# Kernel tuning notes

Hardware: AMD Instinct MI355X
Metric: run time of the kernel (lower is better)

## Reference

```python
import jax, jax.numpy as jnp
import numpy as np

K = 5          # reassembly kernel size
S = 2          # scale factor
ENC_PAD = 1    # encoder_kernel_size // 2


def _conv2d(x, w, pad):
    return jax.lax.conv_general_dilated(
        x, w, window_strides=(1, 1), padding=[(pad, pad), (pad, pad)],
        dimension_numbers=('NCHW', 'OIHW', 'NCHW'))


def setup_inputs() -> dict:
    key = jax.random.key(0)
    k1, k2, k3 = jax.random.split(key, 3)
    x = jax.random.normal(k1, (2, 256, 40, 40), dtype=jnp.float32)
    # channel compressor: xavier-uniform-ish 1x1 conv weight (64, 256, 1, 1)
    limit = np.sqrt(6.0 / (256 + 64)).astype(np.float32)
    w_comp = jax.random.uniform(k2, (64, 256, 1, 1), dtype=jnp.float32,
                                minval=-limit, maxval=limit)
    # content encoder: normal(0, 0.001), out = k^2*s^2 = 100 channels
    w_enc = 0.001 * jax.random.normal(k3, (100, 64, 3, 3), dtype=jnp.float32)
    return {"x": x, "w_comp": w_comp, "w_enc": w_enc}


def reference(x, w_comp, w_enc):
    b, c, h, w = x.shape
    k2 = K * K
    h_up, w_up = h * S, w * S

    # --- kernel prediction ---
    compressed = _conv2d(x, w_comp, 0)                # (b, 64, h, w)
    kern = _conv2d(compressed, w_enc, ENC_PAD)        # (b, k2*S^2, h, w)
    # pixel shuffle: (b, k2, S, S, h, w) -> (b, k2, h, S, w, S) -> (b, k2, h_up, w_up)
    kern = kern.reshape(b, k2, S, S, h, w).transpose(0, 1, 4, 2, 5, 3)
    kern = kern.reshape(b, k2, h_up * w_up)
    kern = jax.nn.softmax(kern, axis=1)               # softmax over k2

    # --- unfold (im2col, padding K//2) ---
    pad = K // 2
    xp = jnp.pad(x, ((0, 0), (0, 0), (pad, pad), (pad, pad)))
    # (b, c, k2, h, w): channel-major, kernel offsets inner (matches torch F.unfold)
    patches = jnp.stack([xp[:, :, i:i + h, j:j + w]
                         for i in range(K) for j in range(K)], axis=2)
    x_unfold = patches.reshape(b, c, k2, h * w)

    # --- reassembly (faithful to the torch 'efficient' path) ---
    # torch repeat_interleaves x_unfold S^2 times along the h*w axis and
    # multiplies with kernels flattened in (h_up*w_up) row-major order; that
    # pairing is exactly kern reshaped to (b, k2, h*w, S^2):
    kern4 = kern.reshape(b, k2, h * w, S * S)
    out = jnp.einsum('bckp,bkpd->bcpd', x_unfold, kern4)  # (b, c, h*w, S^2)
    return out.reshape(b, c, h_up, w_up)
```

## Files before the change

### kernel.cpp

```cpp
#include <hip/hip_runtime.h>

#define B   2
#define C   256
#define CM  64
#define CE  100
#define H   40
#define W   40
#define HW  1600
#define KK  25

__global__ __launch_bounds__(256) void k1_fused(
    const float* __restrict__ x, const float* __restrict__ w_comp,
    const float* __restrict__ w_enc, float* __restrict__ pc,
    float* __restrict__ xpad, float* __restrict__ wT) {
  const int bid = blockIdx.x;
  const int tid = threadIdx.x;

  if (bid >= 712) {
    int idx = (bid - 712) * 256 + tid;
    if (idx < 57600) {
      int row = idx / 576, col = idx - row * 576;
      int ocq = row / 25, ol = row - ocq * 25;
      wT[((size_t)(ocq * 576 + col)) * 32 + ol] = w_enc[idx];
    }
    return;
  }
  if (bid >= 200) {
    const int plane = bid - 200;
    const float* src = x + (size_t)plane * HW;
    float* dst = xpad + (size_t)plane * (44 * 48);
    for (int i = tid; i < 44 * 48; i += 256) {
      int py = i / 48, px = i - py * 48;
      int gy = py - 2, gx = px - 2;
      float v = 0.f;
      if (gy >= 0 && gy < H && gx >= 0 && gx < W) v = src[gy * W + gx];
      dst[i] = v;
    }
    return;
  }

  const int t = bid % 25, ich = (bid / 25) & 3, b = bid / 100;
  __shared__ __align__(16) float xs[64 * 64];
  __shared__ __align__(16) float wsA[64 * 64];

  const float4* x4 = (const float4*)(x + ((size_t)b * C + ich * 64) * HW + t * 64);
#pragma unroll
  for (int i = 0; i < 4; i++) {
    int idx = tid + i * 256;
    ((float4*)xs)[idx] = x4[(idx >> 4) * 400 + (idx & 15)];
  }
  const float4* w4 = (const float4*)w_comp;
#pragma unroll
  for (int i = 0; i < 4; i++) {
    int idx = tid + i * 256;
    int icq = idx >> 6, oc = idx & 63;
    float4 f = w4[oc * 64 + ich * 16 + icq];
    wsA[(icq * 4 + 0) * 64 + oc] = f.x;
    wsA[(icq * 4 + 1) * 64 + oc] = f.y;
    wsA[(icq * 4 + 2) * 64 + oc] = f.z;
    wsA[(icq * 4 + 3) * 64 + oc] = f.w;
  }
  __syncthreads();

  const int ty = tid >> 4, tx = tid & 15;
  float acc[4][4];
#pragma unroll
  for (int i = 0; i < 4; i++)
#pragma unroll
    for (int j = 0; j < 4; j++) acc[i][j] = 0.f;

#pragma unroll 4
  for (int icl = 0; icl < 64; icl++) {
    float4 a = *(const float4*)&wsA[icl * 64 + ty * 4];
    float4 bb = *(const float4*)&xs[icl * 64 + tx * 4];
    float av[4] = {a.x, a.y, a.z, a.w};
    float bv[4] = {bb.x, bb.y, bb.z, bb.w};
#pragma unroll
    for (int i = 0; i < 4; i++)
#pragma unroll
      for (int j = 0; j < 4; j++) acc[i][j] += av[i] * bv[j];
  }

  float* o = pc + ((size_t)ich * B + b) * CM * HW + t * 64 + tx * 4;
#pragma unroll
  for (int j = 0; j < 4; j++)
    *(float4*)&o[(size_t)(ty * 4 + j) * HW] =
        make_float4(acc[j][0], acc[j][1], acc[j][2], acc[j][3]);
}

__global__ __launch_bounds__(256) void k2_conv3x3(
    const float* __restrict__ pc, const float* __restrict__ wT,
    float* __restrict__ encP) {
  const int t = blockIdx.x, ocq = blockIdx.y, icq = blockIdx.z;
  const int ty = t / 10, tx = t - ty * 10;
  __shared__ __align__(16) float smem[3200];
  float* cs   = smem;
  float* pacc = smem;
  const int tid = threadIdx.x;

  for (int i = tid; i < 1920; i += 256) {
    int bb = i / 960, r = i - bb * 960;
    int icl = r / 60, rr = r - icl * 60;
    int yy = rr / 6, xx = rr - yy * 6;
    int gy = ty * 8 + yy - 1, gx = tx * 4 + xx - 1;
    float v = 0.f;
    if (gy >= 0 && gy < H && gx >= 0 && gx < W) {
      int o = bb * 102400 + (icq * 16 + icl) * HW + gy * W + gx;
      v = pc[o] + pc[204800 + o] + pc[409600 + o] + pc[614400 + o];
    }
    cs[i] = v;
  }
  __syncthreads();

  const int wv = tid >> 6, lane = tid & 63;
  const int bb = lane >> 5, py = (lane & 31) >> 2, px = lane & 3;
  float acc[25];
#pragma unroll
  for (int j = 0; j < 25; j++) acc[j] = 0.f;

  const float* wbase0 = wT + (size_t)((ocq * 4 + icq) * 16) * 288;

#pragma unroll
  for (int t4 = 0; t4 < 4; t4++) {
    const int icl = __builtin_amdgcn_readfirstlane(wv * 4 + t4);
    const float* c0 = &cs[(bb * 16 + icl) * 60 + py * 6 + px];
    const float* wrow = wbase0 + icl * 288;
#pragma unroll
    for (int dy = 0; dy < 3; dy++)
#pragma unroll
      for (int dx = 0; dx < 3; dx++) {
        const float xv = c0[dy * 6 + dx];
        const float* wq = wrow + (dy * 3 + dx) * 32;
#pragma unroll
        for (int j = 0; j < 25; j++) acc[j] = fmaf(xv, wq[j], acc[j]);
      }
  }

  __syncthreads();
  if (wv == 1 || wv == 3) {
    const int slot = wv >> 1;
#pragma unroll
    for (int j = 0; j < 25; j++) pacc[(slot * 25 + j) * 64 + lane] = acc[j];
  }
  __syncthreads();
  if (wv == 0 || wv == 2) {
    const int slot = wv >> 1;
#pragma unroll
    for (int j = 0; j < 25; j++) acc[j] += pacc[(slot * 25 + j) * 64 + lane];
  }
  __syncthreads();
  if (wv == 2) {
#pragma unroll
    for (int j = 0; j < 25; j++) pacc[j * 64 + lane] = acc[j];
  }
  __syncthreads();
  if (wv == 0) {
    const int base_px = (ty * 8 + py) * W + tx * 4 + px;
#pragma unroll
    for (int ol = 0; ol < 25; ol++)
      encP[(((size_t)icq * 2 + bb) * CE + ocq * 25 + ol) * HW + base_px] =
          acc[ol] + pacc[ol * 64 + lane];
  }
}

__global__ __launch_bounds__(256) void k3_fused(
    const float* __restrict__ xpad, const float* __restrict__ encP,
    float* __restrict__ out) {
  const int i0 = blockIdx.x;
  const int jq = blockIdx.y;
  const int b  = blockIdx.z;
  const int tid = threadIdx.x;

  __shared__ __align__(16) float xsm[40 * 260];
  __shared__ __align__(16) float sv[400];
  __shared__ __align__(16) float wlds[400];

  const int t20 = (jq >= 5) ? 1 : 0;
  if (tid < 200) {
    const float* eb = encP + (size_t)b * 160000 + i0 * 40;
#pragma unroll
    for (int u = 0; u < 2; u++) {
      const int p = tid * 2 + u;
      const int k = p >> 4, v = p & 15;
      const int j0l = v >> 2, d = v & 3;
      const int off = 2 * t20 + (d & 1);
      const int col = (jq * 4 + j0l - 20 * t20) * 2 + (d >> 1);
      const float* ep = eb + (size_t)(k * 4 + off) * 1600 + col;
      sv[p] = ep[0] + ep[320000] + ep[640000] + ep[960000];
    }
  }

  {
    const float* xb = xpad + (size_t)b * 256 * (44 * 48) + i0 * 48 + jq * 4;
    const int f4 = tid & 1, cth = tid >> 1;
#pragma unroll
    for (int it = 0; it < 10; it++) {
      const int ki = (it < 5) ? it : it - 5;
      const int c  = (it < 5 ? 0 : 128) + cth;
      float4 v = *(const float4*)(xb + ((size_t)c * 44 + ki) * 48 + f4 * 4);
      const int px = ki * 8 + f4 * 4;
      xsm[(px + 0) * 260 + c] = v.x;
      xsm[(px + 1) * 260 + c] = v.y;
      xsm[(px + 2) * 260 + c] = v.z;
      xsm[(px + 3) * 260 + c] = v.w;
    }
  }
  __syncthreads();

  if (tid < 16) {
    const int j0l = tid >> 2, d = tid & 3;
    float vk[KK];
    float m = -1e30f;
#pragma unroll
    for (int k = 0; k < KK; k++) {
      vk[k] = sv[k * 16 + tid];
      m = fmaxf(m, vk[k]);
    }
    float s = 0.f;
#pragma unroll
    for (int k = 0; k < KK; k++) {
      vk[k] = expf(vk[k] - m);
      s += vk[k];
    }
    const float inv = 1.f / s;
#pragma unroll
    for (int k = 0; k < KK; k++) wlds[j0l * 100 + k * 4 + d] = vk[k] * inv;
  }
  __syncthreads();

  const int wv = tid >> 6, lane = tid & 63, ch0 = lane * 4;
  float4 a0 = make_float4(0.f, 0.f, 0.f, 0.f);
  float4 a1 = a0, a2 = a0, a3 = a0;

#pragma unroll
  for (int ki = 0; ki < 5; ki++)
#pragma unroll
    for (int kj = 0; kj < 5; kj++) {
      float4 xv = *(const float4*)&xsm[(ki * 8 + wv + kj) * 260 + ch0];
      float4 w4 = *(const float4*)&wlds[wv * 100 + (ki * 5 + kj) * 4];
      a0.x += xv.x * w4.x; a0.y += xv.y * w4.x; a0.z += xv.z * w4.x; a0.w += xv.w * w4.x;
      a1.x += xv.x * w4.y; a1.y += xv.y * w4.y; a1.z += xv.z * w4.y; a1.w += xv.w * w4.y;
      a2.x += xv.x * w4.z; a2.y += xv.y * w4.z; a2.z += xv.z * w4.z; a2.w += xv.w * w4.z;
      a3.x += xv.x * w4.w; a3.y += xv.y * w4.w; a3.z += xv.z * w4.w; a3.w += xv.w * w4.w;
    }

  const int j0 = jq * 4 + wv;
  float* ob = out + ((size_t)b * C + ch0) * 6400 + i0 * 160 + j0 * 4;
  *(float4*)&ob[0]     = make_float4(a0.x, a1.x, a2.x, a3.x);
  *(float4*)&ob[6400]  = make_float4(a0.y, a1.y, a2.y, a3.y);
  *(float4*)&ob[12800] = make_float4(a0.z, a1.z, a2.z, a3.z);
  *(float4*)&ob[19200] = make_float4(a0.w, a1.w, a2.w, a3.w);
}

extern "C" void kernel_launch(void* const* d_in, const int* in_sizes, int n_in,
                              void* d_out, int out_size, void* d_ws, size_t ws_size,
                              hipStream_t stream) {
  const float* x      = (const float*)d_in[0];
  const float* w_comp = (const float*)d_in[1];
  const float* w_enc  = (const float*)d_in[2];
  float* out = (float*)d_out;

  float* pc    = (float*)d_ws;
  float* encP  = (float*)((char*)d_ws + 3276800);
  float* wT    = (float*)((char*)d_ws + 8396800);
  float* xpad  = (float*)((char*)d_ws + 8691712);

  k1_fused<<<dim3(937), 256, 0, stream>>>(x, w_comp, w_enc, pc, xpad, wT);
  k2_conv3x3<<<dim3(50, 4, 4), 256, 0, stream>>>(pc, wT, encP);
  k3_fused<<<dim3(40, 10, B), 256, 0, stream>>>(xpad, encP, out);
}
```

Baseline: 103.4 us.

## Fuse three kernels into one persistent kernel with atomic grid barriers

Merges the compressor/pad/weight-transpose, 3x3 encoder conv, and softmax-reassembly kernels into a single persistent kernel of 400 blocks. Blocks loop over virtual block indices and meet at atomic-counter grid barriers between stages. A memset resets the barrier counters on each call. The aim is to remove the launch gaps between kernels, at the cost of spin-wait barriers, a deadlock risk if not all blocks are co-resident, and a larger shared-memory footprint that may lower occupancy.

```diff
diff --git a/kernel.cpp b/kernel.cpp
--- a/kernel.cpp
+++ b/kernel.cpp
@@ -9,247 +9,259 @@
 #define HW  1600
 #define KK  25
 
-__global__ __launch_bounds__(256) void k1_fused(
+#define NBLK 400u
+
+__device__ __forceinline__ void grid_barrier(unsigned* cnt) {
+  __syncthreads();
+  if (threadIdx.x == 0) {
+    __hip_atomic_fetch_add(cnt, 1u, __ATOMIC_RELEASE, __HIP_MEMORY_SCOPE_AGENT);
+    while (__hip_atomic_load(cnt, __ATOMIC_ACQUIRE, __HIP_MEMORY_SCOPE_AGENT) <
+           NBLK)
+      __builtin_amdgcn_s_sleep(2);
+  }
+  __syncthreads();
+}
+
+__global__ __launch_bounds__(256) void k_all(
     const float* __restrict__ x, const float* __restrict__ w_comp,
     const float* __restrict__ w_enc, float* __restrict__ pc,
-    float* __restrict__ xpad, float* __restrict__ wT) {
+    float* __restrict__ encP, float* __restrict__ wT,
+    float* __restrict__ xpad, float* __restrict__ out,
+    unsigned* __restrict__ bars) {
+  __shared__ __align__(16) float smem[11200];
   const int bid = blockIdx.x;
   const int tid = threadIdx.x;
 
-  if (bid >= 712) {
-    int idx = (bid - 712) * 256 + tid;
-    if (idx < 57600) {
-      int row = idx / 576, col = idx - row * 576;
-      int ocq = row / 25, ol = row - ocq * 25;
-      wT[((size_t)(ocq * 576 + col)) * 32 + ol] = w_enc[idx];
-    }
-    return;
-  }
-  if (bid >= 200) {
-    const int plane = bid - 200;
-    const float* src = x + (size_t)plane * HW;
-    float* dst = xpad + (size_t)plane * (44 * 48);
-    for (int i = tid; i < 44 * 48; i += 256) {
-      int py = i / 48, px = i - py * 48;
-      int gy = py - 2, gx = px - 2;
+  for (int vb = bid; vb < 937; vb += NBLK) {
+    if (vb >= 712) {
+      int idx = (vb - 712) * 256 + tid;
+      if (idx < 57600) {
+        int row = idx / 576, col = idx - row * 576;
+        int ocq = row / 25, ol = row - ocq * 25;
+        wT[((size_t)(ocq * 576 + col)) * 32 + ol] = w_enc[idx];
+      }
+    } else if (vb >= 200) {
+      const int plane = vb - 200;
+      const float* src = x + (size_t)plane * HW;
+      float* dst = xpad + (size_t)plane * (44 * 48);
+      for (int i = tid; i < 44 * 48; i += 256) {
+        int py = i / 48, px = i - py * 48;
+        int gy = py - 2, gx = px - 2;
+        float v = 0.f;
+        if (gy >= 0 && gy < H && gx >= 0 && gx < W) v = src[gy * W + gx];
+        dst[i] = v;
+      }
+    } else {
+      const int t = vb % 25, ich = (vb / 25) & 3, b = vb / 100;
+      float* xs  = smem;
+      float* wsA = smem + 4096;
+
+      const float4* x4 =
+          (const float4*)(x + ((size_t)b * C + ich * 64) * HW + t * 64);
+#pragma unroll
+      for (int i = 0; i < 4; i++) {
+        int idx = tid + i * 256;
+        ((float4*)xs)[idx] = x4[(idx >> 4) * 400 + (idx & 15)];
+      }
+      const float4* w4 = (const float4*)w_comp;
+#pragma unroll
+      for (int i = 0; i < 4; i++) {
+        int idx = tid + i * 256;
+        int icq = idx >> 6, oc = idx & 63;
+        float4 f = w4[oc * 64 + ich * 16 + icq];
+        wsA[(icq * 4 + 0) * 64 + oc] = f.x;
+        wsA[(icq * 4 + 1) * 64 + oc] = f.y;
+        wsA[(icq * 4 + 2) * 64 + oc] = f.z;
+        wsA[(icq * 4 + 3) * 64 + oc] = f.w;
+      }
+      __syncthreads();
+
+      const int ty = tid >> 4, tx = tid & 15;
+      float acc[4][4];
+#pragma unroll
+      for (int i = 0; i < 4; i++)
+#pragma unroll
+        for (int j = 0; j < 4; j++) acc[i][j] = 0.f;
+
+#pragma unroll 4
+      for (int icl = 0; icl < 64; icl++) {
+        float4 a = *(const float4*)&wsA[icl * 64 + ty * 4];
+        float4 bb = *(const float4*)&xs[icl * 64 + tx * 4];
+        float av[4] = {a.x, a.y, a.z, a.w};
+        float bv[4] = {bb.x, bb.y, bb.z, bb.w};
+#pragma unroll
+        for (int i = 0; i < 4; i++)
+#pragma unroll
+          for (int j = 0; j < 4; j++) acc[i][j] += av[i] * bv[j];
+      }
+
+      float* o = pc + ((size_t)ich * B + b) * CM * HW + t * 64 + tx * 4;
+#pragma unroll
+      for (int j = 0; j < 4; j++)
+        *(float4*)&o[(size_t)(ty * 4 + j) * HW] =
+            make_float4(acc[j][0], acc[j][1], acc[j][2], acc[j][3]);
+    }
+  }
+
+  grid_barrier(&bars[0]);
+
+  for (int vb = bid; vb < 800; vb += NBLK) {
+    __syncthreads();
+    const int t = vb % 50, ocq = (vb / 50) % 4, icq = vb / 200;
+    const int ty = t / 10, tx = t - ty * 10;
+    float* cs   = smem;
+    float* pacc = smem;
+
+    for (int i = tid; i < 1920; i += 256) {
+      int bb = i / 960, r = i - bb * 960;
+      int icl = r / 60, rr = r - icl * 60;
+      int yy = rr / 6, xx = rr - yy * 6;
+      int gy = ty * 8 + yy - 1, gx = tx * 4 + xx - 1;
       float v = 0.f;
-      if (gy >= 0 && gy < H && gx >= 0 && gx < W) v = src[gy * W + gx];
-      dst[i] = v;
-    }
-    return;
-  }
-
-  const int t = bid % 25, ich = (bid / 25) & 3, b = bid / 100;
-  __shared__ __align__(16) float xs[64 * 64];
-  __shared__ __align__(16) float wsA[64 * 64];
-
-  const float4* x4 = (const float4*)(x + ((size_t)b * C + ich * 64) * HW + t * 64);
-#pragma unroll
-  for (int i = 0; i < 4; i++) {
-    int idx = tid + i * 256;
-    ((float4*)xs)[idx] = x4[(idx >> 4) * 400 + (idx & 15)];
-  }
-  const float4* w4 = (const float4*)w_comp;
-#pragma unroll
-  for (int i = 0; i < 4; i++) {
-    int idx = tid + i * 256;
-    int icq = idx >> 6, oc = idx & 63;
-    float4 f = w4[oc * 64 + ich * 16 + icq];
-    wsA[(icq * 4 + 0) * 64 + oc] = f.x;
-    wsA[(icq * 4 + 1) * 64 + oc] = f.y;
-    wsA[(icq * 4 + 2) * 64 + oc] = f.z;
-    wsA[(icq * 4 + 3) * 64 + oc] = f.w;
-  }
-  __syncthreads();
-
-  const int ty = tid >> 4, tx = tid & 15;
-  float acc[4][4];
-#pragma unroll
-  for (int i = 0; i < 4; i++)
-#pragma unroll
-    for (int j = 0; j < 4; j++) acc[i][j] = 0.f;
-
-#pragma unroll 4
-  for (int icl = 0; icl < 64; icl++) {
-    float4 a = *(const float4*)&wsA[icl * 64 + ty * 4];
-    float4 bb = *(const float4*)&xs[icl * 64 + tx * 4];
-    float av[4] = {a.x, a.y, a.z, a.w};
-    float bv[4] = {bb.x, bb.y, bb.z, bb.w};
-#pragma unroll
-    for (int i = 0; i < 4; i++)
-#pragma unroll
-      for (int j = 0; j < 4; j++) acc[i][j] += av[i] * bv[j];
-  }
-
-  float* o = pc + ((size_t)ich * B + b) * CM * HW + t * 64 + tx * 4;
-#pragma unroll
-  for (int j = 0; j < 4; j++)
-    *(float4*)&o[(size_t)(ty * 4 + j) * HW] =
-        make_float4(acc[j][0], acc[j][1], acc[j][2], acc[j][3]);
-}
-
-__global__ __launch_bounds__(256) void k2_conv3x3(
-    const float* __restrict__ pc, const float* __restrict__ wT,
-    float* __restrict__ encP) {
-  const int t = blockIdx.x, ocq = blockIdx.y, icq = blockIdx.z;
-  const int ty = t / 10, tx = t - ty * 10;
-  __shared__ __align__(16) float smem[3200];
-  float* cs   = smem;
-  float* pacc = smem;
-  const int tid = threadIdx.x;
-
-  for (int i = tid; i < 1920; i += 256) {
-    int bb = i / 960, r = i - bb * 960;
-    int icl = r / 60, rr = r - icl * 60;
-    int yy = rr / 6, xx = rr - yy * 6;
-    int gy = ty * 8 + yy - 1, gx = tx * 4 + xx - 1;
-    float v = 0.f;
-    if (gy >= 0 && gy < H && gx >= 0 && gx < W) {
-      int o = bb * 102400 + (icq * 16 + icl) * HW + gy * W + gx;
-      v = pc[o] + pc[204800 + o] + pc[409600 + o] + pc[614400 + o];
-    }
-    cs[i] = v;
-  }
-  __syncthreads();
-
-  const int wv = tid >> 6, lane = tid & 63;
-  const int bb = lane >> 5, py = (lane & 31) >> 2, px = lane & 3;
-  float acc[25];
-#pragma unroll
-  for (int j = 0; j < 25; j++) acc[j] = 0.f;
-
-  const float* wbase0 = wT + (size_t)((ocq * 4 + icq) * 16) * 288;
-
-#pragma unroll
-  for (int t4 = 0; t4 < 4; t4++) {
-    const int icl = __builtin_amdgcn_readfirstlane(wv * 4 + t4);
-    const float* c0 = &cs[(bb * 16 + icl) * 60 + py * 6 + px];
-    const float* wrow = wbase0 + icl * 288;
-#pragma unroll
-    for (int dy = 0; dy < 3; dy++)
-#pragma unroll
-      for (int dx = 0; dx < 3; dx++) {
-        const float xv = c0[dy * 6 + dx];
-        const float* wq = wrow + (dy * 3 + dx) * 32;
-#pragma unroll
-        for (int j = 0; j < 25; j++) acc[j] = fmaf(xv, wq[j], acc[j]);
-      }
-  }
-
-  __syncthreads();
-  if (wv == 1 || wv == 3) {
-    const int slot = wv >> 1;
-#pragma unroll
-    for (int j = 0; j < 25; j++) pacc[(slot * 25 + j) * 64 + lane] = acc[j];
-  }
-  __syncthreads();
-  if (wv == 0 || wv == 2) {
-    const int slot = wv >> 1;
-#pragma unroll
-    for (int j = 0; j < 25; j++) acc[j] += pacc[(slot * 25 + j) * 64 + lane];
-  }
-  __syncthreads();
-  if (wv == 2) {
-#pragma unroll
-    for (int j = 0; j < 25; j++) pacc[j * 64 + lane] = acc[j];
-  }
-  __syncthreads();
-  if (wv == 0) {
-    const int base_px = (ty * 8 + py) * W + tx * 4 + px;
-#pragma unroll
-    for (int ol = 0; ol < 25; ol++)
-      encP[(((size_t)icq * 2 + bb) * CE + ocq * 25 + ol) * HW + base_px] =
-          acc[ol] + pacc[ol * 64 + lane];
-  }
-}
-
-__global__ __launch_bounds__(256) void k3_fused(
-    const float* __restrict__ xpad, const float* __restrict__ encP,
-    float* __restrict__ out) {
-  const int i0 = blockIdx.x;
-  const int jq = blockIdx.y;
-  const int b  = blockIdx.z;
-  const int tid = threadIdx.x;
-
-  __shared__ __align__(16) float xsm[40 * 260];
-  __shared__ __align__(16) float sv[400];
-  __shared__ __align__(16) float wlds[400];
-
-  const int t20 = (jq >= 5) ? 1 : 0;
-  if (tid < 200) {
-    const float* eb = encP + (size_t)b * 160000 + i0 * 40;
-#pragma unroll
-    for (int u = 0; u < 2; u++) {
-      const int p = tid * 2 + u;
-      const int k = p >> 4, v = p & 15;
-      const int j0l = v >> 2, d = v & 3;
-      const int off = 2 * t20 + (d & 1);
-      const int col = (jq * 4 + j0l - 20 * t20) * 2 + (d >> 1);
-      const float* ep = eb + (size_t)(k * 4 + off) * 1600 + col;
-      sv[p] = ep[0] + ep[320000] + ep[640000] + ep[960000];
-    }
-  }
-
-  {
-    const float* xb = xpad + (size_t)b * 256 * (44 * 48) + i0 * 48 + jq * 4;
-    const int f4 = tid & 1, cth = tid >> 1;
-#pragma unroll
-    for (int it = 0; it < 10; it++) {
-      const int ki = (it < 5) ? it : it - 5;
-      const int c  = (it < 5 ? 0 : 128) + cth;
-      float4 v = *(const float4*)(xb + ((size_t)c * 44 + ki) * 48 + f4 * 4);
-      const int px = ki * 8 + f4 * 4;
-      xsm[(px + 0) * 260 + c] = v.x;
-      xsm[(px + 1) * 260 + c] = v.y;
-      xsm[(px + 2) * 260 + c] = v.z;
-      xsm[(px + 3) * 260 + c] = v.w;
-    }
-  }
-  __syncthreads();
-
-  if (tid < 16) {
-    const int j0l = tid >> 2, d = tid & 3;
-    float vk[KK];
-    float m = -1e30f;
-#pragma unroll
-    for (int k = 0; k < KK; k++) {
-      vk[k] = sv[k * 16 + tid];
-      m = fmaxf(m, vk[k]);
-    }
-    float s = 0.f;
-#pragma unroll
-    for (int k = 0; k < KK; k++) {
-      vk[k] = expf(vk[k] - m);
-      s += vk[k];
-    }
-    const float inv = 1.f / s;
-#pragma unroll
-    for (int k = 0; k < KK; k++) wlds[j0l * 100 + k * 4 + d] = vk[k] * inv;
-  }
-  __syncthreads();
-
-  const int wv = tid >> 6, lane = tid & 63, ch0 = lane * 4;
-  float4 a0 = make_float4(0.f, 0.f, 0.f, 0.f);
-  float4 a1 = a0, a2 = a0, a3 = a0;
-
-#pragma unroll
-  for (int ki = 0; ki < 5; ki++)
-#pragma unroll
-    for (int kj = 0; kj < 5; kj++) {
-      float4 xv = *(const float4*)&xsm[(ki * 8 + wv + kj) * 260 + ch0];
-      float4 w4 = *(const float4*)&wlds[wv * 100 + (ki * 5 + kj) * 4];
-      a0.x += xv.x * w4.x; a0.y += xv.y * w4.x; a0.z += xv.z * w4.x; a0.w += xv.w * w4.x;
-      a1.x += xv.x * w4.y; a1.y += xv.y * w4.y; a1.z += xv.z * w4.y; a1.w += xv.w * w4.y;
-      a2.x += xv.x * w4.z; a2.y += xv.y * w4.z; a2.z += xv.z * w4.z; a2.w += xv.w * w4.z;
-      a3.x += xv.x * w4.w; a3.y += xv.y * w4.w; a3.z += xv.z * w4.w; a3.w += xv.w * w4.w;
-    }
-
-  const int j0 = jq * 4 + wv;
-  float* ob = out + ((size_t)b * C + ch0) * 6400 + i0 * 160 + j0 * 4;
-  *(float4*)&ob[0]     = make_float4(a0.x, a1.x, a2.x, a3.x);
-  *(float4*)&ob[6400]  = make_float4(a0.y, a1.y, a2.y, a3.y);
-  *(float4*)&ob[12800] = make_float4(a0.z, a1.z, a2.z, a3.z);
-  *(float4*)&ob[19200] = make_float4(a0.w, a1.w, a2.w, a3.w);
+      if (gy >= 0 && gy < H && gx >= 0 && gx < W) {
+        int o = bb * 102400 + (icq * 16 + icl) * HW + gy * W + gx;
+        v = pc[o] + pc[204800 + o] + pc[409600 + o] + pc[614400 + o];
+      }
+      cs[i] = v;
+    }
+    __syncthreads();
+
+    const int wv = tid >> 6, lane = tid & 63;
+    const int bb = lane >> 5, py = (lane & 31) >> 2, px = lane & 3;
+    float acc[25];
+#pragma unroll
+    for (int j = 0; j < 25; j++) acc[j] = 0.f;
+
+    const float* wbase0 = wT + (size_t)((ocq * 4 + icq) * 16) * 288;
+
+#pragma unroll
+    for (int t4 = 0; t4 < 4; t4++) {
+      const int icl = __builtin_amdgcn_readfirstlane(wv * 4 + t4);
+      const float* c0 = &cs[(bb * 16 + icl) * 60 + py * 6 + px];
+      const float* wrow = wbase0 + icl * 288;
+#pragma unroll
+      for (int dy = 0; dy < 3; dy++)
+#pragma unroll
+        for (int dx = 0; dx < 3; dx++) {
+          const float xv = c0[dy * 6 + dx];
+          const float* wq = wrow + (dy * 3 + dx) * 32;
+#pragma unroll
+          for (int j = 0; j < 25; j++) acc[j] = fmaf(xv, wq[j], acc[j]);
+        }
+    }
+
+    __syncthreads();
+    if (wv == 1 || wv == 3) {
+      const int slot = wv >> 1;
+#pragma unroll
+      for (int j = 0; j < 25; j++) pacc[(slot * 25 + j) * 64 + lane] = acc[j];
+    }
+    __syncthreads();
+    if (wv == 0 || wv == 2) {
+      const int slot = wv >> 1;
+#pragma unroll
+      for (int j = 0; j < 25; j++) acc[j] += pacc[(slot * 25 + j) * 64 + lane];
+    }
+    __syncthreads();
+    if (wv == 2) {
+#pragma unroll
+      for (int j = 0; j < 25; j++) pacc[j * 64 + lane] = acc[j];
+    }
+    __syncthreads();
+    if (wv == 0) {
+      const int base_px = (ty * 8 + py) * W + tx * 4 + px;
+#pragma unroll
+      for (int ol = 0; ol < 25; ol++)
+        encP[(((size_t)icq * 2 + bb) * CE + ocq * 25 + ol) * HW + base_px] =
+            acc[ol] + pacc[ol * 64 + lane];
+    }
+  }
+
+  grid_barrier(&bars[1]);
+
+  for (int vb = bid; vb < 800; vb += NBLK) {
+    __syncthreads();
+    const int i0 = vb % 40, jq = (vb / 40) % 10, b = vb / 400;
+    float* xsm  = smem;
+    float* sv   = smem + 10400;
+    float* wlds = smem + 10800;
+
+    const int t20 = (jq >= 5) ? 1 : 0;
+    if (tid < 200) {
+      const float* eb = encP + (size_t)b * 160000 + i0 * 40;
+#pragma unroll
+      for (int u = 0; u < 2; u++) {
+        const int p = tid * 2 + u;
+        const int k = p >> 4, v = p & 15;
+        const int j0l = v >> 2, d = v & 3;
+        const int off = 2 * t20 + (d & 1);
+        const int col = (jq * 4 + j0l - 20 * t20) * 2 + (d >> 1);
+        const float* ep = eb + (size_t)(k * 4 + off) * 1600 + col;
+        sv[p] = ep[0] + ep[320000] + ep[640000] + ep[960000];
+      }
+    }
+
+    {
+      const float* xb = xpad + (size_t)b * 256 * (44 * 48) + i0 * 48 + jq * 4;
+      const int f4 = tid & 1, cth = tid >> 1;
+#pragma unroll
+      for (int it = 0; it < 10; it++) {
+        const int ki = (it < 5) ? it : it - 5;
+        const int c  = (it < 5 ? 0 : 128) + cth;
+        float4 v = *(const float4*)(xb + ((size_t)c * 44 + ki) * 48 + f4 * 4);
+        const int px = ki * 8 + f4 * 4;
+        xsm[(px + 0) * 260 + c] = v.x;
+        xsm[(px + 1) * 260 + c] = v.y;
+        xsm[(px + 2) * 260 + c] = v.z;
+        xsm[(px + 3) * 260 + c] = v.w;
+      }
+    }
+    __syncthreads();
+
+    if (tid < 16) {
+      const int j0l = tid >> 2, d = tid & 3;
+      float vk[KK];
+      float m = -1e30f;
+#pragma unroll
+      for (int k = 0; k < KK; k++) {
+        vk[k] = sv[k * 16 + tid];
+        m = fmaxf(m, vk[k]);
+      }
+      float s = 0.f;
+#pragma unroll
+      for (int k = 0; k < KK; k++) {
+        vk[k] = expf(vk[k] - m);
+        s += vk[k];
+      }
+      const float inv = 1.f / s;
+#pragma unroll
+      for (int k = 0; k < KK; k++) wlds[j0l * 100 + k * 4 + d] = vk[k] * inv;
+    }
+    __syncthreads();
+
+    const int wv = tid >> 6, lane = tid & 63, ch0 = lane * 4;
+    float4 a0 = make_float4(0.f, 0.f, 0.f, 0.f);
+    float4 a1 = a0, a2 = a0, a3 = a0;
+
+#pragma unroll
+    for (int ki = 0; ki < 5; ki++)
+#pragma unroll
+      for (int kj = 0; kj < 5; kj++) {
+        float4 xv = *(const float4*)&xsm[(ki * 8 + wv + kj) * 260 + ch0];
+        float4 w4 = *(const float4*)&wlds[wv * 100 + (ki * 5 + kj) * 4];
+        a0.x += xv.x * w4.x; a0.y += xv.y * w4.x; a0.z += xv.z * w4.x; a0.w += xv.w * w4.x;
+        a1.x += xv.x * w4.y; a1.y += xv.y * w4.y; a1.z += xv.z * w4.y; a1.w += xv.w * w4.y;
+        a2.x += xv.x * w4.z; a2.y += xv.y * w4.z; a2.z += xv.z * w4.z; a2.w += xv.w * w4.z;
+        a3.x += xv.x * w4.w; a3.y += xv.y * w4.w; a3.z += xv.z * w4.w; a3.w += xv.w * w4.w;
+      }
+
+    const int j0 = jq * 4 + wv;
+    float* ob = out + ((size_t)b * C + ch0) * 6400 + i0 * 160 + j0 * 4;
+    *(float4*)&ob[0]     = make_float4(a0.x, a1.x, a2.x, a3.x);
+    *(float4*)&ob[6400]  = make_float4(a0.y, a1.y, a2.y, a3.y);
+    *(float4*)&ob[12800] = make_float4(a0.z, a1.z, a2.z, a3.z);
+    *(float4*)&ob[19200] = make_float4(a0.w, a1.w, a2.w, a3.w);
+  }
 }
 
 extern "C" void kernel_launch(void* const* d_in, const int* in_sizes, int n_in,
@@ -260,12 +272,14 @@
   const float* w_enc  = (const float*)d_in[2];
   float* out = (float*)d_out;
 
-  float* pc    = (float*)d_ws;
-  float* encP  = (float*)((char*)d_ws + 3276800);
-  float* wT    = (float*)((char*)d_ws + 8396800);
-  float* xpad  = (float*)((char*)d_ws + 8691712);
-
-  k1_fused<<<dim3(937), 256, 0, stream>>>(x, w_comp, w_enc, pc, xpad, wT);
-  k2_conv3x3<<<dim3(50, 4, 4), 256, 0, stream>>>(pc, wT, encP);
-  k3_fused<<<dim3(40, 10, B), 256, 0, stream>>>(xpad, encP, out);
+  float* pc       = (float*)d_ws;
+  float* encP     = (float*)((char*)d_ws + 3276800);
+  float* wT       = (float*)((char*)d_ws + 8396800);
+  float* xpad     = (float*)((char*)d_ws + 8691712);
+  unsigned* bars  = (unsigned*)((char*)d_ws + 16000000);
+
+  hipMemsetAsync(bars, 0, 2 * sizeof(unsigned), stream);
+
+  k_all<<<dim3(NBLK), dim3(256), 0, stream>>>(x, w_comp, w_enc, pc, encP, wT,
+                                              xpad, out, bars);
 }
```

After: 268.1 us. +159.4%, slower.
